# Performance work log

Measured on AMD Instinct MI355X. Metric: run time of the kernel, lower is better.

The kernel has to match this reference:

```python
import jax, jax.numpy as jnp
import numpy as np

B_IMG, T_PER, DIN = 8, 4096, 1176
D, E, BN, L, TOP_K, OUT = 1024, 8, 64, 4, 2, 4096


def setup_inputs() -> dict:
    key = jax.random.key(0)
    ks = jax.random.split(key, 16)
    s = 0.02
    inp = {
        "pixel_values": jax.random.normal(ks[0], (B_IMG * T_PER, DIN), jnp.float32),
        "image_grid_thw": jnp.tile(jnp.array([[1, 64, 64]], dtype=jnp.int64), (B_IMG, 1)),
        # in_proj (no bias)
        "w_in": jax.random.normal(ks[1], (DIN, D), jnp.float32) * s,
        # skin classifier: Linear(D,64) -> ReLU -> Linear(64,3)
        "w_sc1": jax.random.normal(ks[2], (D, 64), jnp.float32) * s,
        "b_sc1": jnp.zeros((64,), jnp.float32),
        "w_sc2": jax.random.normal(ks[3], (64, 3), jnp.float32) * s,
        "b_sc2": jnp.zeros((3,), jnp.float32),
        # per-adapter-layer routers (stacked over L)
        "w_rimg": jax.random.normal(ks[4], (L, D, E), jnp.float32) * s,
        "w_rskin": jax.random.normal(ks[5], (L, 3, E), jnp.float32) * s,
        # per-layer, per-expert MLP: Linear(D,BN) -> ReLU -> Linear(BN,D)
        "ew1": jax.random.normal(ks[6], (L, E, D, BN), jnp.float32) * s,
        "eb1": jnp.zeros((L, E, BN), jnp.float32),
        "ew2": jax.random.normal(ks[7], (L, E, BN, D), jnp.float32) * s,
        "eb2": jnp.zeros((L, E, D), jnp.float32),
        # out_proj
        "w_out": jax.random.normal(ks[8], (D, OUT), jnp.float32) * s,
        "b_out": jnp.zeros((OUT,), jnp.float32),
    }
    return inp


def _forward(pixel_values, image_grid_thw, w_in, w_sc1, b_sc1, w_sc2, b_sc2,
             w_rimg, w_rskin, ew1, eb1, ew2, eb2, w_out, b_out):
    B = image_grid_thw.shape[0]
    T = pixel_values.shape[0] // B  # equal chunk sizes (t*h*w identical per image)
    x = pixel_values.reshape(B, T, -1)

    def per_image(xc):  # xc: [T, din]
        h = xc @ w_in  # [T, D]
        g = h.mean(0)
        skin_logits = jax.nn.relu(g @ w_sc1 + b_sc1) @ w_sc2 + b_sc2  # [3]
        skin_probs = jax.nn.softmax(skin_logits)

        def layer(carry, params):
            h, aux = carry
            wri, wrs, W1, B1, W2, B2 = params
            logits = h @ wri + skin_probs @ wrs  # [T, E]
            probs = jax.nn.softmax(logits, axis=-1)
            tp, ti = jax.lax.top_k(probs, TOP_K)
            tp = tp / (tp.sum(-1, keepdims=True) + 1e-6)
            rows = jnp.arange(h.shape[0])[:, None]
            # dense per-token expert weights (0 for non-selected experts)
            wfull = jnp.zeros_like(probs).at[rows, ti].add(tp)
            mask = jnp.zeros_like(probs).at[rows, ti].add(1.0)
            h1 = jax.nn.relu(jnp.einsum('td,edb->teb', h, W1) + B1)  # [T,E,BN]
            h2 = jnp.einsum('teb,ebd->ted', h1, W2) + B2             # [T,E,D]
            moe_out = jnp.einsum('ted,te->td', h2, wfull)
            aux = aux + (probs.mean(0) * mask.mean(0)).sum() * probs.shape[-1]
            return (h + moe_out, aux), None

        (h, aux), _ = jax.lax.scan(layer, (h, jnp.zeros((), h.dtype)),
                                   (w_rimg, w_rskin, ew1, eb1, ew2, eb2))
        return h.mean(0), skin_logits, aux

    pooled, skin_logits, aux = jax.vmap(per_image)(x)
    vision_proj = pooled @ w_out + b_out
    return pooled, vision_proj, aux.sum(), skin_logits


def reference(pixel_values, image_grid_thw, w_in, w_sc1, b_sc1, w_sc2, b_sc2,
              w_rimg, w_rskin, ew1, eb1, ew2, eb2, w_out, b_out):
    return _forward(pixel_values, image_grid_thw, w_in, w_sc1, b_sc1, w_sc2, b_sc2,
                    w_rimg, w_rskin, ew1, eb1, ew2, eb2, w_out, b_out)
```

## Files before the change

kernel.cpp:

```cpp
#include <hip/hip_runtime.h>
#include <math.h>

#define TPI  4096
#define TT   32768
#define DIN  1176
#define KP   1216
#define DM   1024
#define NE   8
#define BN   64
#define NL   4
#define DOUT 4096
#define TBLK 32

typedef __attribute__((ext_vector_type(4))) float floatx4;
typedef __attribute__((ext_vector_type(8))) short bf16x8;
typedef unsigned int uint;

__device__ inline short f2bf(float x) {
    unsigned u = __float_as_uint(x);
    u += 0x7fffu + ((u >> 16) & 1u);
    return (short)(u >> 16);
}
__device__ inline float bf2f(short h) {
    return __uint_as_float(((unsigned)(unsigned short)h) << 16);
}

#define GLP(p) ((const __attribute__((address_space(1))) void*)(p))
#define LDSP(p) ((__attribute__((address_space(3))) void*)(p))
#define ASYNC16(g, s) __builtin_amdgcn_global_load_lds(GLP(g), LDSP(s), 16, 0, 0)

#define OFF_H0    0ul
#define OFF_H1    67108864ul
#define OFF_XB    67108864ul
#define OFF_WBT   146800640ul
#define OFF_E1T   149291008ul
#define OFF_E2T   153485312ul
#define OFF_BTOK  157679616ul
#define OFF_BW1   157810688ul
#define OFF_BW2   157941760ul
#define OFF_T2E   158072832ul
#define OFF_T2W   158203904ul
#define OFF_Z     158466048ul
#define Z_BYTES   39232ul
#define OFF_RB    158505280ul
#define OFF_WRT   158506304ul

__global__ __launch_bounds__(256) void convx_kernel(
    const float* __restrict__ X, short* __restrict__ Xb)
{
    const long row = blockIdx.x;
    const float* src = X + row * (long)DIN;
    short* dst = Xb + row * (long)KP;
    for (int i = threadIdx.x; i < 304; i += 256) {
        short4 s;
        if (i < 294) {
            float4 v = *(const float4*)(src + i * 4);
            s.x = f2bf(v.x); s.y = f2bf(v.y); s.z = f2bf(v.z); s.w = f2bf(v.w);
        } else {
            s.x = 0; s.y = 0; s.z = 0; s.w = 0;
        }
        *(short4*)(dst + i * 4) = s;
    }
}

__global__ __launch_bounds__(256) void transp_kernel(
    const float* __restrict__ src, short* __restrict__ dst, int RS, int CS, int DK)
{
    __shared__ float tb[64][65];
    const int kt = blockIdx.x * 64, nt = blockIdx.y * 64;
    const long sb = (long)blockIdx.z * RS * CS;
    const long db = (long)blockIdx.z * CS * DK;
    const int rr = threadIdx.x >> 6, cc = threadIdx.x & 63;
#pragma unroll
    for (int i = 0; i < 16; ++i) {
        int r = i * 4 + rr;
        int k = kt + r, n = nt + cc;
        tb[r][cc] = (k < RS && n < CS) ? src[sb + (long)k * CS + n] : 0.0f;
    }
    __syncthreads();
#pragma unroll
    for (int i = 0; i < 16; ++i) {
        int r = i * 4 + rr;
        int n = nt + r, k = kt + cc;
        if (n < CS && k < DK) dst[db + (long)n * DK + k] = f2bf(tb[cc][r]);
    }
}

__global__ __launch_bounds__(256) void wrt_kernel(
    const float* __restrict__ w_rimg, short* __restrict__ wrT)
{
    const int l = blockIdx.x >> 4, e = blockIdx.x & 15;
    short* dst = wrT + ((long)l * 16 + e) * 1024;
    if (e < 8) {
        const float* src = w_rimg + (long)l * 8192 + e;
        for (int k = threadIdx.x; k < 1024; k += 256) dst[k] = f2bf(src[k * 8]);
    } else {
        for (int k = threadIdx.x; k < 1024; k += 256) dst[k] = 0;
    }
}

__global__ __launch_bounds__(256) void gemm_in_mfma(
    const short* __restrict__ Xb, const short* __restrict__ Wbt,
    short* __restrict__ Hb, float* __restrict__ g)
{
    __shared__ __align__(16) short As[128 * 64];
    __shared__ __align__(16) short Bs[128 * 64];
    const int tid = threadIdx.x;
    const int m0 = blockIdx.x * 128, n0 = blockIdx.y * 128;
    const int w = tid >> 6, lane = tid & 63;
    const int quad = lane >> 4, l15 = lane & 15;
    const int wm = (w >> 1) * 64, wn = (w & 1) * 64;

    floatx4 acc[4][4];
#pragma unroll
    for (int i = 0; i < 4; ++i)
#pragma unroll
        for (int j = 0; j < 4; ++j) acc[i][j] = 0.0f;

    const int r = tid >> 3;
    const int gofs = ((tid & 7) ^ (r & 7)) * 8;
    const short* ap = Xb + (long)(m0 + r) * KP + gofs;
    const short* bp = Wbt + (long)(n0 + r) * KP + gofs;
    short* asd = As + tid * 8;
    short* bsd = Bs + tid * 8;
    const int rx = l15 & 7;

    for (int k0 = 0; k0 < KP; k0 += 64) {
        __syncthreads();
#pragma unroll
        for (int i = 0; i < 4; ++i) {
            ASYNC16(ap + (long)i * 32 * KP + k0, asd + i * 2048);
            ASYNC16(bp + (long)i * 32 * KP + k0, bsd + i * 2048);
        }
        __syncthreads();
#pragma unroll
        for (int kk = 0; kk < 2; ++kk) {
            bf16x8 af[4], bfr[4];
#pragma unroll
            for (int i = 0; i < 4; ++i)
                af[i] = *(const bf16x8*)&As[(wm + i * 16 + l15) * 64 + (((kk * 4 + quad)) ^ rx) * 8];
#pragma unroll
            for (int j = 0; j < 4; ++j)
                bfr[j] = *(const bf16x8*)&Bs[(wn + j * 16 + l15) * 64 + (((kk * 4 + quad)) ^ rx) * 8];
#pragma unroll
            for (int i = 0; i < 4; ++i)
#pragma unroll
                for (int j = 0; j < 4; ++j)
                    acc[i][j] = __builtin_amdgcn_mfma_f32_16x16x32_bf16(af[i], bfr[j], acc[i][j], 0, 0, 0);
        }
    }
    const int img = m0 >> 12;
#pragma unroll
    for (int j = 0; j < 4; ++j) {
        float cs = 0.0f;
#pragma unroll
        for (int i = 0; i < 4; ++i)
#pragma unroll
            for (int r2 = 0; r2 < 4; ++r2) {
                short hv = f2bf(acc[i][j][r2]);
                Hb[(long)(m0 + wm + i * 16 + quad * 4 + r2) * DM + n0 + wn + j * 16 + l15] =
                    hv;
                cs += bf2f(hv);
            }
        cs += __shfl_xor(cs, 16);
        cs += __shfl_xor(cs, 32);
        if (quad == 0)
            atomicAdd(&g[img * DM + n0 + wn + j * 16 + l15], cs * (1.0f / 4096.0f));
    }
}

__global__ __launch_bounds__(256) void colmean_kernel(
    const short* __restrict__ Hb, float* __restrict__ outp)
{
    const int col = blockIdx.x * 256 + threadIdx.x;
    const int img = blockIdx.y;
    const int t0 = blockIdx.z * 256;
    const short* p = Hb + ((long)img * TPI + t0) * DM + col;
    float s = 0.0f;
#pragma unroll 8
    for (int t = 0; t < 256; ++t) s += bf2f(p[(long)t * DM]);
    atomicAdd(&outp[img * DM + col], s * (1.0f / 4096.0f));
}

__global__ __launch_bounds__(256) void skin1_kernel(
    const float* __restrict__ g, const float* __restrict__ w_sc1,
    const float* __restrict__ b_sc1, float* __restrict__ hsg)
{
    __shared__ float red[4][64];
    const int img = blockIdx.x;
    const int part = threadIdx.x >> 6, c = threadIdx.x & 63;
    float s = 0.0f;
    for (int i = 0; i < 256; ++i) {
        int d = part * 256 + i;
        s += g[img * DM + d] * w_sc1[d * 64 + c];
    }
    red[part][c] = s;
    __syncthreads();
    if (part == 0) {
        float v = red[0][c] + red[1][c] + red[2][c] + red[3][c] + b_sc1[c];
        hsg[img * 64 + c] = fmaxf(v, 0.0f);
    }
}

__global__ __launch_bounds__(256) void skin2_kernel(
    const float* __restrict__ hsg, const float* __restrict__ w_sc2, const float* __restrict__ b_sc2,
    const float* __restrict__ w_rskin, float* __restrict__ skin_logits_out, float* __restrict__ rb)
{
    __shared__ float l3[24];
    __shared__ float sp[24];
    const int tid = threadIdx.x;
    if (tid < 24) {
        int img = tid / 3, j = tid % 3;
        float s = b_sc2[j];
        for (int c = 0; c < 64; ++c) s += hsg[img * 64 + c] * w_sc2[c * 3 + j];
        l3[tid] = s;
        skin_logits_out[tid] = s;
    }
    __syncthreads();
    if (tid < 8) {
        float v0 = l3[tid * 3], v1 = l3[tid * 3 + 1], v2 = l3[tid * 3 + 2];
        float m = fmaxf(v0, fmaxf(v1, v2));
        float e0 = expf(v0 - m), e1 = expf(v1 - m), e2 = expf(v2 - m);
        float inv = 1.0f / (e0 + e1 + e2);
        sp[tid * 3] = e0 * inv; sp[tid * 3 + 1] = e1 * inv; sp[tid * 3 + 2] = e2 * inv;
    }
    __syncthreads();
    {
        int l = tid >> 6, img = (tid >> 3) & 7, e = tid & 7;
        float s = 0.0f;
#pragma unroll
        for (int c = 0; c < 3; ++c) s += sp[img * 3 + c] * w_rskin[(l * 3 + c) * 8 + e];
        rb[tid] = s;
    }
}

__global__ __launch_bounds__(256) void router_kernel(
    const short* __restrict__ Hb, const short* __restrict__ wrT, const float* __restrict__ rb,
    uint* __restrict__ top2e, float* __restrict__ top2w, int* __restrict__ counts_pair,
    float* __restrict__ sum_probs, float* __restrict__ mask_cnt, int l)
{
    __shared__ __align__(16) short As[8 * 64 * 32];
    __shared__ float lgS[64 * 9];
    const int tid = threadIdx.x;
    const int tok0 = blockIdx.x * 64;
    const int img = tok0 >> 12;
    const int w = tid >> 6, lane = tid & 63;
    const int quad = lane >> 4, l15 = lane & 15;

    const short* rowptr = Hb + (long)(tok0 + w * 16 + (lane >> 2)) * DM + (lane & 3) * 8;
    short* sdst = As + tid * 8;
    const short* wrl = wrT + (long)l * 16 * 1024 + l15 * 1024 + quad * 8;

    floatx4 acc = 0.0f;
    for (int k0 = 0; k0 < DM; k0 += 256) {
        __syncthreads();
#pragma unroll
        for (int c = 0; c < 8; ++c) ASYNC16(rowptr + k0 + c * 32, sdst + c * 2048);
        __syncthreads();
#pragma unroll
        for (int c = 0; c < 8; ++c) {
            bf16x8 af = *(const bf16x8*)&As[c * 2048 + (w * 16 + l15) * 32 + quad * 8];
            bf16x8 bf = *(const bf16x8*)(wrl + k0 + c * 32);
            acc = __builtin_amdgcn_mfma_f32_16x16x32_bf16(af, bf, acc, 0, 0, 0);
        }
    }
    if (l15 < 8) {
#pragma unroll
        for (int r = 0; r < 4; ++r) lgS[(w * 16 + quad * 4 + r) * 9 + l15] = acc[r];
    }
    __syncthreads();

    if (tid < 64) {
        const int token = tok0 + tid;
        float p[8];
        float mx = -1e30f;
#pragma unroll
        for (int e = 0; e < 8; ++e) {
            float v = lgS[tid * 9 + e] + rb[l * 64 + img * 8 + e];
            p[e] = v; mx = fmaxf(mx, v);
        }
        float s = 0.0f;
#pragma unroll
        for (int e = 0; e < 8; ++e) { p[e] = expf(p[e] - mx); s += p[e]; }
        float inv = 1.0f / s;
#pragma unroll
        for (int e = 0; e < 8; ++e) p[e] *= inv;

        int i1 = 0; float b1v = p[0];
#pragma unroll
        for (int e = 1; e < 8; ++e) if (p[e] > b1v) { b1v = p[e]; i1 = e; }
        int i2 = -1; float b2v = -1.0f;
#pragma unroll
        for (int e = 0; e < 8; ++e) if (e != i1 && p[e] > b2v) { b2v = p[e]; i2 = e; }
        float den = b1v + b2v + 1e-6f;
        top2e[token] = (uint)i1 | ((uint)i2 << 8);
        top2w[2 * token] = b1v / den;
        top2w[2 * token + 1] = b2v / den;

        atomicAdd(&counts_pair[l * 64 + i1 * 8 + i2], 1);

        for (int slot = 0; slot < 2; ++slot) {
            int esel = slot ? i2 : i1;
#pragma unroll
            for (int e = 0; e < 8; ++e) {
                unsigned long long m = __ballot(esel == e);
                int pc = __popcll(m);
                if (pc && tid == (__ffsll(m) - 1))
                    atomicAdd(&mask_cnt[l * 64 + img * 8 + e], (float)pc);
            }
        }
#pragma unroll
        for (int e = 0; e < 8; ++e) {
            float rsum = p[e];
            for (int off = 32; off > 0; off >>= 1) rsum += __shfl_down(rsum, off);
            if (tid == 0) atomicAdd(&sum_probs[l * 64 + img * 8 + e], rsum);
        }
    }
}

__global__ __launch_bounds__(256) void scatter_kernel(
    const uint* __restrict__ top2e, const float* __restrict__ top2w,
    const int* __restrict__ counts_pair, int* __restrict__ cursors,
    int* __restrict__ btok, float* __restrict__ bw1, float* __restrict__ bw2, int l)
{
    __shared__ int pofS[64];
    const int tid = threadIdx.x;
    if (tid < 64) {
        int c = counts_pair[l * 64 + tid];
        int x = c;
#pragma unroll
        for (int off = 1; off < 64; off <<= 1) {
            int y = __shfl_up(x, off);
            if (tid >= off) x += y;
        }
        pofS[tid] = x - c;
    }
    __syncthreads();
    const int t = blockIdx.x * 256 + tid;
    const int lane = tid & 63;
    uint pe = top2e[t];
    int p = (int)(pe & 255u) * 8 + (int)((pe >> 8) & 255u);
    float w1 = top2w[2 * t], w2 = top2w[2 * t + 1];
    int myoff = pofS[p];
    unsigned long long rem = __ballot(true);
    while (rem) {
        int leader = __ffsll(rem) - 1;
        int pv = __shfl(p, leader);
        unsigned long long m = __ballot(p == pv);
        int basep = 0;
        if (lane == leader) basep = atomicAdd(&cursors[l * 64 + pv], __popcll(m));
        basep = __shfl(basep, leader);
        if (p == pv) {
            int pos = basep + __popcll(m & ((1ull << lane) - 1ull));
            int s = myoff + pos;
            btok[s] = t;
            bw1[s] = w1;
            bw2[s] = w2;
        }
        rem &= ~m;
    }
}

__global__ __launch_bounds__(256, 4) void expert_pair(
    const short* __restrict__ Hin, short* __restrict__ Hout,
    int* __restrict__ counts_pair,
    const int* __restrict__ btok, const float* __restrict__ bw1, const float* __restrict__ bw2,
    const short* __restrict__ ew1t, const float* __restrict__ eb1,
    const short* __restrict__ ew2t, const float* __restrict__ eb2,
    const short* __restrict__ wrT, const float* __restrict__ rb,
    uint* __restrict__ top2e, float* __restrict__ top2w,
    float* __restrict__ sum_probs, float* __restrict__ mask_cnt, int l)
{
    __shared__ __align__(16) short As[TBLK * 256];
    __shared__ __align__(16) short h1ab[2][TBLK * 72];
    __shared__ int tkS[TBLK];
    __shared__ float w1S[TBLK], w2S[TBLK];
    __shared__ int pofS[64], cntS[64], tpS[64];
    __shared__ int nworkS;
    __shared__ float spLDS[64], mkLDS[64];

    short* h1a = &h1ab[0][0];
    short* h1b = &h1ab[1][0];
    float* lgF = (float*)&h1ab[0][0];

    const int tid = threadIdx.x;
    const int w = tid >> 6, lane = tid & 63;
    const int quad = lane >> 4, l15 = lane & 15;

    if (tid < 64) {
        int c = counts_pair[l * 64 + tid];
        cntS[tid] = c;
        int x = c;
#pragma unroll
        for (int off = 1; off < 64; off <<= 1) {
            int y = __shfl_up(x, off);
            if (tid >= off) x += y;
        }
        pofS[tid] = x - c;
        int nb = (c + TBLK - 1) >> 5;
        int t = nb;
#pragma unroll
        for (int off = 1; off < 64; off <<= 1) {
            int y = __shfl_up(t, off);
            if (tid >= off) t += y;
        }
        tpS[tid] = t;
        if (tid == 63) nworkS = t;
    }
    __syncthreads();
    const int nwork = nworkS;

    for (int wi = blockIdx.x; wi < nwork; wi += gridDim.x) {
        int p = 0;
        while (p < 63 && tpS[p] <= wi) ++p;
        const int cnt = cntS[p];
        const int nbp = (cnt + TBLK - 1) >> 5;
        const int base = (wi - (tpS[p] - nbp)) * TBLK;
        const int ea = p >> 3, eb = p & 7;
        const int off = pofS[p];
        const int lea = l * 8 + ea, leb = l * 8 + eb;

        __syncthreads();
        if (tid < TBLK) {
            bool valid = (base + tid) < cnt;
            int s = off + base + tid;
            tkS[tid] = valid ? btok[s] : 0;
            w1S[tid] = valid ? bw1[s] : 0.0f;
            w2S[tid] = valid ? bw2[s] : 0.0f;
        }
        if (tid < 64) { spLDS[tid] = 0.0f; mkLDS[tid] = 0.0f; }
        __syncthreads();

        const int srow[4] = { tid >> 5, 8 + (tid >> 5), 16 + (tid >> 5), 24 + (tid >> 5) };
        const int sj = tid & 31;

        floatx4 acc1a[2], acc1b[2];
#pragma unroll
        for (int i = 0; i < 2; ++i) { acc1a[i] = 0.0f; acc1b[i] = 0.0f; }
        const short* w1ap = ew1t + ((long)lea * BN + w * 16 + l15) * DM + quad * 8;
        const short* w1bp = ew1t + ((long)leb * BN + w * 16 + l15) * DM + quad * 8;

        for (int k0 = 0; k0 < DM; k0 += 256) {
            __syncthreads();
#pragma unroll
            for (int cc = 0; cc < 4; ++cc) {
                const int row = srow[cc];
                const short* src = Hin + (long)tkS[row] * DM + k0 + ((sj ^ (row & 7)) << 3);
                ASYNC16(src, As + (cc * 256 + tid) * 8);
            }
            __syncthreads();
#pragma unroll
            for (int c = 0; c < 8; ++c) {
                bf16x8 ba = *(const bf16x8*)(w1ap + k0 + c * 32);
                bf16x8 bb = *(const bf16x8*)(w1bp + k0 + c * 32);
#pragma unroll
                for (int i = 0; i < 2; ++i) {
                    const int tok = i * 16 + l15;
                    bf16x8 af = *(const bf16x8*)&As[tok * 256 + (((c * 4 + quad) ^ (tok & 7)) << 3)];
                    acc1a[i] = __builtin_amdgcn_mfma_f32_16x16x32_bf16(af, ba, acc1a[i], 0, 0, 0);
                    acc1b[i] = __builtin_amdgcn_mfma_f32_16x16x32_bf16(af, bb, acc1b[i], 0, 0, 0);
                }
            }
        }
        {
            float b1av = eb1[lea * BN + w * 16 + l15];
            float b1bv = eb1[leb * BN + w * 16 + l15];
#pragma unroll
            for (int i = 0; i < 2; ++i)
#pragma unroll
                for (int r = 0; r < 4; ++r) {
                    h1a[(i * 16 + quad * 4 + r) * 72 + w * 16 + l15] =
                        f2bf(fmaxf(acc1a[i][r] + b1av, 0.0f));
                    h1b[(i * 16 + quad * 4 + r) * 72 + w * 16 + l15] =
                        f2bf(fmaxf(acc1b[i][r] + b1bv, 0.0f));
                }
        }
        __syncthreads();

        bf16x8 hra[2][2], hrb[2][2];
#pragma unroll
        for (int kk = 0; kk < 2; ++kk)
#pragma unroll
            for (int tj = 0; tj < 2; ++tj) {
                hra[kk][tj] = *(const bf16x8*)&h1a[(tj * 16 + l15) * 72 + kk * 32 + quad * 8];
                hrb[kk][tj] = *(const bf16x8*)&h1b[(tj * 16 + l15) * 72 + kk * 32 + quad * 8];
            }

        const short* w2ap = ew2t + ((long)lea * DM + w * 16 + l15) * 64 + quad * 8;
        const short* w2bp = ew2t + ((long)leb * DM + w * 16 + l15) * 64 + quad * 8;
        const short* wrp = wrT + ((long)(l + 1 < NL ? l + 1 : 0) * 16 + l15) * 1024 + quad * 8;

        floatx4 acc_lg[2];
#pragma unroll
        for (int tf = 0; tf < 2; ++tf) acc_lg[tf] = 0.0f;

        for (int gidx = 0; gidx < 4; ++gidx) {
            const int g0 = gidx * 256;
            __syncthreads();
#pragma unroll
            for (int cc = 0; cc < 4; ++cc) {
                const int row = srow[cc];
                const short* src = Hin + (long)tkS[row] * DM + g0 + ((sj ^ (row & 7)) << 3);
                ASYNC16(src, As + (cc * 256 + tid) * 8);
            }
            __syncthreads();
#pragma unroll
            for (int ns = 0; ns < 4; ++ns) {
                const int n0 = g0 + ns * 64;
                floatx4 a2a[2], a2b[2];
#pragma unroll
                for (int tj = 0; tj < 2; ++tj) { a2a[tj] = 0.0f; a2b[tj] = 0.0f; }
#pragma unroll
                for (int kk = 0; kk < 2; ++kk) {
                    bf16x8 wa = *(const bf16x8*)(w2ap + (long)n0 * 64 + kk * 32);
                    bf16x8 wb = *(const bf16x8*)(w2bp + (long)n0 * 64 + kk * 32);
#pragma unroll
                    for (int tj = 0; tj < 2; ++tj) {
                        a2a[tj] = __builtin_amdgcn_mfma_f32_16x16x32_bf16(wa, hra[kk][tj], a2a[tj], 0, 0, 0);
                        a2b[tj] = __builtin_amdgcn_mfma_f32_16x16x32_bf16(wb, hrb[kk][tj], a2b[tj], 0, 0, 0);
                    }
                }
                const int nloc = ns * 64 + w * 16 + quad * 4;
                const int jch = nloc >> 3, jof = nloc & 7;
                float4 b2av = *(const float4*)&eb2[lea * DM + g0 + nloc];
                float4 b2bv = *(const float4*)&eb2[leb * DM + g0 + nloc];
#pragma unroll
                for (int tj = 0; tj < 2; ++tj) {
                    int tk = tj * 16 + l15;
                    float w1v = w1S[tk], w2v = w2S[tk];
                    short* slot = &As[tk * 256 + ((jch ^ (tk & 7)) << 3) + jof];
                    short4 res = *(short4*)slot;
                    short4 o;
                    o.x = f2bf(bf2f(res.x) + w1v * (a2a[tj][0] + b2av.x) + w2v * (a2b[tj][0] + b2bv.x));
                    o.y = f2bf(bf2f(res.y) + w1v * (a2a[tj][1] + b2av.y) + w2v * (a2b[tj][1] + b2bv.y));
                    o.z = f2bf(bf2f(res.z) + w1v * (a2a[tj][2] + b2av.z) + w2v * (a2b[tj][2] + b2bv.z));
                    o.w = f2bf(bf2f(res.w) + w1v * (a2a[tj][3] + b2av.w) + w2v * (a2b[tj][3] + b2bv.w));
                    *(short4*)slot = o;
                }
            }
            __syncthreads();

            if (l < 3) {
#pragma unroll
                for (int kk = 0; kk < 2; ++kk) {
                    const int c = w * 2 + kk;
                    bf16x8 wf = *(const bf16x8*)(wrp + g0 + c * 32);
#pragma unroll
                    for (int tf = 0; tf < 2; ++tf) {
                        const int tok = tf * 16 + l15;
                        bf16x8 of = *(const bf16x8*)&As[tok * 256 + (((c * 4 + quad) ^ (tok & 7)) << 3)];
                        acc_lg[tf] = __builtin_amdgcn_mfma_f32_16x16x32_bf16(wf, of, acc_lg[tf], 0, 0, 0);
                    }
                }
            }
#pragma unroll
            for (int cc = 0; cc < 4; ++cc) {
                const int row = srow[cc];
                if ((base + row) < cnt) {
                    int4 v = *(const int4*)&As[row * 256 + ((sj ^ (row & 7)) << 3)];
                    *(int4*)(Hout + (long)tkS[row] * DM + g0 + (sj << 3)) = v;
                }
            }
        }

        if (l < 3) {
            __syncthreads();
#pragma unroll
            for (int tf = 0; tf < 2; ++tf)
                *(floatx4*)&lgF[(w * 32 + tf * 16 + l15) * 16 + quad * 4] = acc_lg[tf];
            __syncthreads();
            if (tid < TBLK) {
                const bool valid = (base + tid) < cnt;
                const int token = tkS[tid];
                const int img = token >> 12;
                float pb[8]; float mx = -1e30f;
#pragma unroll
                for (int e = 0; e < 8; ++e) {
                    float v = lgF[tid * 16 + e] + lgF[(32 + tid) * 16 + e]
                            + lgF[(64 + tid) * 16 + e] + lgF[(96 + tid) * 16 + e]
                            + rb[(l + 1) * 64 + img * 8 + e];
                    pb[e] = v; mx = fmaxf(mx, v);
                }
                float s = 0.0f;
#pragma unroll
                for (int e = 0; e < 8; ++e) { pb[e] = expf(pb[e] - mx); s += pb[e]; }
                float inv = 1.0f / s;
#pragma unroll
                for (int e = 0; e < 8; ++e) pb[e] *= inv;
                int i1 = 0; float b1v = pb[0];
#pragma unroll
                for (int e = 1; e < 8; ++e) if (pb[e] > b1v) { b1v = pb[e]; i1 = e; }
                int i2 = -1; float b2v = -1.0f;
#pragma unroll
                for (int e = 0; e < 8; ++e) if (e != i1 && pb[e] > b2v) { b2v = pb[e]; i2 = e; }
                if (valid) {
                    float den = b1v + b2v + 1e-6f;
                    top2e[token] = (uint)i1 | ((uint)i2 << 8);
                    top2w[2 * token] = b1v / den;
                    top2w[2 * token + 1] = b2v / den;
                    atomicAdd(&counts_pair[(l + 1) * 64 + i1 * 8 + i2], 1);
#pragma unroll
                    for (int e = 0; e < 8; ++e) atomicAdd(&spLDS[img * 8 + e], pb[e]);
                    atomicAdd(&mkLDS[img * 8 + i1], 1.0f);
                    atomicAdd(&mkLDS[img * 8 + i2], 1.0f);
                }
            }
            __syncthreads();
            if (tid < 64) {
                float v = spLDS[tid];
                if (v != 0.0f) atomicAdd(&sum_probs[(l + 1) * 64 + tid], v);
                float mz = mkLDS[tid];
                if (mz != 0.0f) atomicAdd(&mask_cnt[(l + 1) * 64 + tid], mz);
            }
        }
    }
}

__global__ __launch_bounds__(256) void vproj_kernel(
    const float* __restrict__ pooled, const float* __restrict__ w_out,
    const float* __restrict__ b_out, float* __restrict__ outp)
{
    __shared__ float ps[8 * 128];
    const int tid = threadIdx.x;
    const int n = blockIdx.x * 256 + tid;
    const int d0 = blockIdx.y * 128;
#pragma unroll
    for (int i = 0; i < 4; ++i) {
        int idx = tid + i * 256;
        ps[idx] = pooled[(idx >> 7) * DM + d0 + (idx & 127)];
    }
    __syncthreads();
    float acc[8];
    float binit = (blockIdx.y == 0) ? b_out[n] : 0.0f;
#pragma unroll
    for (int img = 0; img < 8; ++img) acc[img] = binit;
    for (int d = 0; d < 128; ++d) {
        float wv = w_out[(long)(d0 + d) * DOUT + n];
#pragma unroll
        for (int img = 0; img < 8; ++img) acc[img] += ps[img * 128 + d] * wv;
    }
#pragma unroll
    for (int img = 0; img < 8; ++img) atomicAdd(&outp[img * DOUT + n], acc[img]);
}

__global__ __launch_bounds__(64) void aux_kernel(
    const float* __restrict__ sum_probs, const float* __restrict__ mask_cnt,
    float* __restrict__ outp)
{
    const int tid = threadIdx.x;
    float v = 0.0f;
    if (tid < 32) {
        float s = 0.0f;
#pragma unroll
        for (int e = 0; e < 8; ++e) s += sum_probs[tid * 8 + e] * mask_cnt[tid * 8 + e];
        v = s * (8.0f / (4096.0f * 4096.0f));
    }
    for (int off = 32; off > 0; off >>= 1) v += __shfl_down(v, off);
    if (tid == 0) outp[0] = v;
}

extern "C" void kernel_launch(void* const* d_in, const int* in_sizes, int n_in,
                              void* d_out, int out_size, void* d_ws, size_t ws_size,
                              hipStream_t stream) {
    const float* X       = (const float*)d_in[0];
    const float* w_in    = (const float*)d_in[2];
    const float* w_sc1   = (const float*)d_in[3];
    const float* b_sc1   = (const float*)d_in[4];
    const float* w_sc2   = (const float*)d_in[5];
    const float* b_sc2   = (const float*)d_in[6];
    const float* w_rimg  = (const float*)d_in[7];
    const float* w_rskin = (const float*)d_in[8];
    const float* ew1     = (const float*)d_in[9];
    const float* eb1     = (const float*)d_in[10];
    const float* ew2     = (const float*)d_in[11];
    const float* eb2     = (const float*)d_in[12];
    const float* w_out   = (const float*)d_in[13];
    const float* b_out   = (const float*)d_in[14];

    float* out = (float*)d_out;
    char* ws = (char*)d_ws;

    short* H0   = (short*)(ws + OFF_H0);
    short* H1   = (short*)(ws + OFF_H1);
    short* Xb   = (short*)(ws + OFF_XB);
    short* Wbt  = (short*)(ws + OFF_WBT);
    short* ew1t = (short*)(ws + OFF_E1T);
    short* ew2t = (short*)(ws + OFF_E2T);
    int*   btok = (int*)(ws + OFF_BTOK);
    float* bw1  = (float*)(ws + OFF_BW1);
    float* bw2  = (float*)(ws + OFF_BW2);
    uint*  top2e = (uint*)(ws + OFF_T2E);
    float* top2w = (float*)(ws + OFF_T2W);
    int*   counts_pair = (int*)(ws + OFF_Z);
    int*   cursors     = (int*)(ws + OFF_Z + 1024);
    float* sum_probs   = (float*)(ws + OFF_Z + 2368);
    float* mask_cnt    = (float*)(ws + OFF_Z + 3392);
    float* g           = (float*)(ws + OFF_Z + 4416);
    float* hsg         = (float*)(ws + OFF_Z + 37184);
    float* rb          = (float*)(ws + OFF_RB);
    short* wrT         = (short*)(ws + OFF_WRT);

    hipMemsetAsync(d_out, 0, (size_t)out_size * sizeof(float), stream);
    hipMemsetAsync(ws + OFF_Z, 0, Z_BYTES, stream);

    dim3 b256(256);
    convx_kernel<<<TT, b256, 0, stream>>>(X, Xb);
    transp_kernel<<<dim3(19, 16, 1), b256, 0, stream>>>(w_in, Wbt, DIN, DM, KP);
    transp_kernel<<<dim3(16, 1, 32), b256, 0, stream>>>(ew1, ew1t, DM, BN, DM);
    transp_kernel<<<dim3(1, 16, 32), b256, 0, stream>>>(ew2, ew2t, BN, DM, BN);
    wrt_kernel<<<64, b256, 0, stream>>>(w_rimg, wrT);
    gemm_in_mfma<<<dim3(256, 8), b256, 0, stream>>>(Xb, Wbt, H0, g);
    skin1_kernel<<<8, b256, 0, stream>>>(g, w_sc1, b_sc1, hsg);
    skin2_kernel<<<1, b256, 0, stream>>>(hsg, w_sc2, b_sc2, w_rskin, out + 40961, rb);
    router_kernel<<<512, b256, 0, stream>>>(H0, wrT, rb, top2e, top2w,
                                            counts_pair, sum_probs, mask_cnt, 0);

    short* Hc = H0;
    short* Hn = H1;
    for (int l = 0; l < NL; ++l) {
        scatter_kernel<<<128, b256, 0, stream>>>(top2e, top2w, counts_pair, cursors,
                                                 btok, bw1, bw2, l);
        expert_pair<<<1152, b256, 0, stream>>>(Hc, Hn, counts_pair, btok, bw1, bw2,
                                               ew1t, eb1, ew2t, eb2, wrT, rb,
                                               top2e, top2w, sum_probs, mask_cnt, l);
        short* tmp = Hc; Hc = Hn; Hn = tmp;
    }
    colmean_kernel<<<dim3(4, 8, 16), b256, 0, stream>>>(Hc, out);
    vproj_kernel<<<dim3(16, 8), b256, 0, stream>>>(out, w_out, b_out, out + 8192);
    aux_kernel<<<1, 64, 0, stream>>>(sum_probs, mask_cnt, out + 40960);
}
```

Measured before the change: 1.525 ms.

## Double-buffer token tiles in LDS for expert_pair and swizzle block work order

The shared token tile is split into two buffers, so the async global-to-LDS copy for the next 256-column chunk is issued before the MFMA work on the current chunk. This overlaps memory latency with compute in both the first-layer and second-layer expert GEMM phases and removes one barrier per chunk. The last chunk of phase one already prefetches the first chunk of phase two. Token row offsets are now read from global memory straight into registers. Work items are also swizzled across blocks, and launch bounds drop to 3 waves per SIMD to fit the doubled LDS, trading occupancy for overlap. The swizzle assumes the grid size is a multiple of 8.

```diff
diff --git a/kernel.cpp b/kernel.cpp
--- a/kernel.cpp
+++ b/kernel.cpp
@@ -361,7 +361,7 @@
     }
 }
 
-__global__ __launch_bounds__(256, 4) void expert_pair(
+__global__ __launch_bounds__(256, 3) void expert_pair(
     const short* __restrict__ Hin, short* __restrict__ Hout,
     int* __restrict__ counts_pair,
     const int* __restrict__ btok, const float* __restrict__ bw1, const float* __restrict__ bw2,
@@ -371,7 +371,7 @@
     uint* __restrict__ top2e, float* __restrict__ top2w,
     float* __restrict__ sum_probs, float* __restrict__ mask_cnt, int l)
 {
-    __shared__ __align__(16) short As[TBLK * 256];
+    __shared__ __align__(16) short As[2][TBLK * 256];
     __shared__ __align__(16) short h1ab[2][TBLK * 72];
     __shared__ int tkS[TBLK];
     __shared__ float w1S[TBLK], w2S[TBLK];
@@ -410,7 +410,12 @@
     __syncthreads();
     const int nwork = nworkS;
 
-    for (int wi = blockIdx.x; wi < nwork; wi += gridDim.x) {
+    const int bswz = (int)((blockIdx.x & 7) * (gridDim.x >> 3) + (blockIdx.x >> 3));
+
+    const int srow0 = tid >> 5;
+    const int sj = tid & 31;
+
+    for (int wi = bswz; wi < nwork; wi += gridDim.x) {
         int p = 0;
         while (p < 63 && tpS[p] <= wi) ++p;
         const int cnt = cntS[p];
@@ -421,6 +426,14 @@
         const int lea = l * 8 + ea, leb = l * 8 + eb;
 
         __syncthreads();
+
+        long srcrow[4];
+#pragma unroll
+        for (int cc = 0; cc < 4; ++cc) {
+            const int row = cc * 8 + srow0;
+            const int tokr = ((base + row) < cnt) ? btok[off + base + row] : 0;
+            srcrow[cc] = (long)tokr * DM + ((sj ^ (row & 7)) << 3);
+        }
         if (tid < TBLK) {
             bool valid = (base + tid) < cnt;
             int s = off + base + tid;
@@ -429,10 +442,11 @@
             w2S[tid] = valid ? bw2[s] : 0.0f;
         }
         if (tid < 64) { spLDS[tid] = 0.0f; mkLDS[tid] = 0.0f; }
+
+#pragma unroll
+        for (int cc = 0; cc < 4; ++cc)
+            ASYNC16(Hin + srcrow[cc], &As[0][(cc * 256 + tid) * 8]);
         __syncthreads();
-
-        const int srow[4] = { tid >> 5, 8 + (tid >> 5), 16 + (tid >> 5), 24 + (tid >> 5) };
-        const int sj = tid & 31;
 
         floatx4 acc1a[2], acc1b[2];
 #pragma unroll
@@ -440,15 +454,15 @@
         const short* w1ap = ew1t + ((long)lea * BN + w * 16 + l15) * DM + quad * 8;
         const short* w1bp = ew1t + ((long)leb * BN + w * 16 + l15) * DM + quad * 8;
 
-        for (int k0 = 0; k0 < DM; k0 += 256) {
-            __syncthreads();
-#pragma unroll
-            for (int cc = 0; cc < 4; ++cc) {
-                const int row = srow[cc];
-                const short* src = Hin + (long)tkS[row] * DM + k0 + ((sj ^ (row & 7)) << 3);
-                ASYNC16(src, As + (cc * 256 + tid) * 8);
-            }
-            __syncthreads();
+#pragma unroll
+        for (int s = 0; s < 4; ++s) {
+            const int nxt = (s < 3) ? (s + 1) * 256 : 0;
+            short* dst = &As[(s & 1) ^ 1][0];
+#pragma unroll
+            for (int cc = 0; cc < 4; ++cc)
+                ASYNC16(Hin + srcrow[cc] + nxt, dst + (cc * 256 + tid) * 8);
+            const short* cur = &As[s & 1][0];
+            const int k0 = s * 256;
 #pragma unroll
             for (int c = 0; c < 8; ++c) {
                 bf16x8 ba = *(const bf16x8*)(w1ap + k0 + c * 32);
@@ -456,11 +470,12 @@
 #pragma unroll
                 for (int i = 0; i < 2; ++i) {
                     const int tok = i * 16 + l15;
-                    bf16x8 af = *(const bf16x8*)&As[tok * 256 + (((c * 4 + quad) ^ (tok & 7)) << 3)];
+                    bf16x8 af = *(const bf16x8*)&cur[tok * 256 + (((c * 4 + quad) ^ (tok & 7)) << 3)];
                     acc1a[i] = __builtin_amdgcn_mfma_f32_16x16x32_bf16(af, ba, acc1a[i], 0, 0, 0);
                     acc1b[i] = __builtin_amdgcn_mfma_f32_16x16x32_bf16(af, bb, acc1b[i], 0, 0, 0);
                 }
             }
+            __syncthreads();
         }
         {
             float b1av = eb1[lea * BN + w * 16 + l15];
@@ -494,16 +509,16 @@
 #pragma unroll
         for (int tf = 0; tf < 2; ++tf) acc_lg[tf] = 0.0f;
 
+#pragma unroll
         for (int gidx = 0; gidx < 4; ++gidx) {
             const int g0 = gidx * 256;
-            __syncthreads();
-#pragma unroll
-            for (int cc = 0; cc < 4; ++cc) {
-                const int row = srow[cc];
-                const short* src = Hin + (long)tkS[row] * DM + g0 + ((sj ^ (row & 7)) << 3);
-                ASYNC16(src, As + (cc * 256 + tid) * 8);
-            }
-            __syncthreads();
+            if (gidx < 3) {
+                short* dst = &As[(gidx & 1) ^ 1][0];
+#pragma unroll
+                for (int cc = 0; cc < 4; ++cc)
+                    ASYNC16(Hin + srcrow[cc] + (g0 + 256), dst + (cc * 256 + tid) * 8);
+            }
+            short* cur = &As[gidx & 1][0];
 #pragma unroll
             for (int ns = 0; ns < 4; ++ns) {
                 const int n0 = g0 + ns * 64;
@@ -528,7 +543,7 @@
                 for (int tj = 0; tj < 2; ++tj) {
                     int tk = tj * 16 + l15;
                     float w1v = w1S[tk], w2v = w2S[tk];
-                    short* slot = &As[tk * 256 + ((jch ^ (tk & 7)) << 3) + jof];
+                    short* slot = &cur[tk * 256 + ((jch ^ (tk & 7)) << 3) + jof];
                     short4 res = *(short4*)slot;
                     short4 o;
                     o.x = f2bf(bf2f(res.x) + w1v * (a2a[tj][0] + b2av.x) + w2v * (a2b[tj][0] + b2bv.x));
@@ -548,23 +563,23 @@
 #pragma unroll
                     for (int tf = 0; tf < 2; ++tf) {
                         const int tok = tf * 16 + l15;
-                        bf16x8 of = *(const bf16x8*)&As[tok * 256 + (((c * 4 + quad) ^ (tok & 7)) << 3)];
+                        bf16x8 of = *(const bf16x8*)&cur[tok * 256 + (((c * 4 + quad) ^ (tok & 7)) << 3)];
                         acc_lg[tf] = __builtin_amdgcn_mfma_f32_16x16x32_bf16(wf, of, acc_lg[tf], 0, 0, 0);
                     }
                 }
             }
 #pragma unroll
             for (int cc = 0; cc < 4; ++cc) {
-                const int row = srow[cc];
+                const int row = cc * 8 + srow0;
                 if ((base + row) < cnt) {
-                    int4 v = *(const int4*)&As[row * 256 + ((sj ^ (row & 7)) << 3)];
+                    int4 v = *(const int4*)&cur[row * 256 + ((sj ^ (row & 7)) << 3)];
                     *(int4*)(Hout + (long)tkS[row] * DM + g0 + (sj << 3)) = v;
                 }
             }
+            __syncthreads();
         }
 
         if (l < 3) {
-            __syncthreads();
 #pragma unroll
             for (int tf = 0; tf < 2; ++tf)
                 *(floatx4*)&lgF[(w * 32 + tf * 16 + l15) * 16 + quad * 4] = acc_lg[tf];
```

Result: no change. 1.510 ms (-1.0%).
